# Performance work log

Measured on AMD Instinct MI355X. Metric: run time of the kernel, lower is better.

Reference implementation:

```python
import jax, jax.numpy as jnp
import numpy as np

H = 256  # hidden_size
I = 18   # input_size
B = 1024 # batch
T = 1024 # seq_len


def setup_inputs() -> dict:
    key = jax.random.key(0)
    ks = jax.random.split(key, 8)
    scale = 1.0 / np.sqrt(H)  # matches torch GRUCell uniform init scale roughly
    s = lambda k, shape: jax.random.normal(k, shape, dtype=jnp.float32) * scale
    return {
        "x": jax.random.normal(ks[0], (B, T, I), dtype=jnp.float32),
        # layer 0 GRUCell params (gate order r, z, n as in torch)
        "W_ih0": s(ks[1], (3 * H, I)),
        "W_hh0": s(ks[2], (3 * H, H)),
        "b_ih0": jnp.zeros((3 * H,), dtype=jnp.float32),
        "b_hh0": jnp.zeros((3 * H,), dtype=jnp.float32),
        # layer 1 GRUCell params
        "W_ih1": s(ks[3], (3 * H, H)),
        "W_hh1": s(ks[4], (3 * H, H)),
        "b_ih1": jnp.zeros((3 * H,), dtype=jnp.float32),
        "b_hh1": jnp.zeros((3 * H,), dtype=jnp.float32),
        "fc_w": s(ks[5], (1, H)),
        "fc_b": jnp.zeros((1,), dtype=jnp.float32),
    }


def _gru_cell(x, h, W_ih, W_hh, b_ih, b_hh):
    # torch.nn.GRUCell math, gate order (r, z, n)
    gi = x @ W_ih.T + b_ih  # (B, 3H)
    gh = h @ W_hh.T + b_hh  # (B, 3H)
    ir, iz, inn = jnp.split(gi, 3, axis=-1)
    hr, hz, hn = jnp.split(gh, 3, axis=-1)
    r = jax.nn.sigmoid(ir + hr)
    z = jax.nn.sigmoid(iz + hz)
    n = jnp.tanh(inn + r * hn)
    return (1.0 - z) * n + z * h


def reference(x, W_ih0, W_hh0, b_ih0, b_hh0, W_ih1, W_hh1, b_ih1, b_hh1, fc_w, fc_b):
    batch = x.shape[0]
    hid = W_hh0.shape[1]
    h_init = (jnp.zeros((batch, hid), dtype=x.dtype),
              jnp.zeros((batch, hid), dtype=x.dtype))
    xs = jnp.swapaxes(x, 0, 1)  # (T, B, I) for scan over time

    def step(carry, xt):
        h0, h1 = carry
        h0 = _gru_cell(xt, h0, W_ih0, W_hh0, b_ih0, b_hh0)
        h1 = _gru_cell(h0, h1, W_ih1, W_hh1, b_ih1, b_hh1)
        return (h0, h1), None

    (h0, h1), _ = jax.lax.scan(step, h_init, xs)
    return h1 @ fc_w.T + fc_b  # (B, 1)
```

## Files before the change

### kernel.cpp

```cpp
#include <hip/hip_runtime.h>

#define B_ 1024
#define T_ 1024
#define I_ 18
#define H_ 256
#define NCHUNK 16
#define NSLICE 16

typedef _Float16 f16;
typedef _Float16 f16x8 __attribute__((ext_vector_type(8)));
typedef float f32x4 __attribute__((ext_vector_type(4)));

#define MFMA16(a, b, c) __builtin_amdgcn_mfma_f32_16x16x32_f16((a), (b), (c), 0, 0, 0)
#define SB() __builtin_amdgcn_sched_barrier(0)

#define WF_FRAGS 75
#define WF_SLICE (WF_FRAGS * 512)
#define WF_TOTAL (NSLICE * WF_SLICE)
#define H_SLOT (NCHUNK * 8 * 4 * 512)
#define NFLAGS (NCHUNK * 4 * 32)

struct TrueT { static constexpr bool value = true; };
struct FalseT { static constexpr bool value = false; };

__device__ __forceinline__ int hoff(int chunk, int kt, int m) {
  return (((chunk * 8) + kt) * 4 + m) * 512;
}

__global__ void init_ws(f16* __restrict__ hb, int hcount, int* __restrict__ flg) {
  int i = blockIdx.x * blockDim.x + threadIdx.x;
  unsigned* p = (unsigned*)hb;
  for (int k = i; k < hcount / 2; k += gridDim.x * blockDim.x) p[k] = 0u;
  if (i < NFLAGS + 256 + 1) flg[i] = 0;
}

__global__ void prep_weights(const float* __restrict__ Wih0,
                             const float* __restrict__ Whh0,
                             const float* __restrict__ Wih1,
                             const float* __restrict__ Whh1,
                             f16* __restrict__ ws) {
  int tid = blockIdx.x * blockDim.x + threadIdx.x;
  if (tid >= NSLICE * WF_FRAGS * 64) return;
  int lane = tid & 63;
  int f = (tid >> 6) % WF_FRAGS;
  int s = tid / (WF_FRAGS * 64);
  int lrow = lane & 15, lgrp = lane >> 4;
  f16 v[8];
  if (f < 3) {
    int n = f * H_ + s * 16 + lrow;
#pragma unroll
    for (int j = 0; j < 8; ++j) {
      int k = lgrp * 8 + j;
      v[j] = (k < I_) ? (f16)Wih0[n * I_ + k] : (f16)0.f;
    }
  } else {
    int ff;
    const float* W;
    if (f < 27) { ff = f - 3;  W = Whh0; }
    else if (f < 51) { ff = f - 27; W = Wih1; }
    else { ff = f - 51; W = Whh1; }
    int g = ff >> 3, kt = ff & 7;
    int n = g * H_ + s * 16 + lrow;
    int kb = kt * 32 + lgrp * 8;
#pragma unroll
    for (int j = 0; j < 8; ++j) v[j] = (f16)W[n * H_ + kb + j];
  }
  *(f16x8*)(ws + ((size_t)s * WF_SLICE + f * 512 + lane * 8)) = *(f16x8*)v;
}

__device__ __forceinline__ float sigm(float v) {
  return __builtin_amdgcn_rcpf(1.f + __expf(-v));
}
__device__ __forceinline__ float tanh_fast(float v) {
  v = fmaxf(v, -15.f);
  float e = __expf(-2.f * v);
  return (1.f - e) * __builtin_amdgcn_rcpf(1.f + e);
}

template <bool FAST>
__device__ __forceinline__ f16x8 ldh(const f16* p) {
  f16x8 r;
  if (FAST)
    asm volatile("global_load_dwordx4 %0, %1, off nt" : "=&v"(r) : "v"(p));
  else
    asm volatile("global_load_dwordx4 %0, %1, off sc0 sc1" : "=&v"(r) : "v"(p));
  return r;
}
template <bool FAST>
__device__ __forceinline__ void sth(f16* p, f16 v) {
  unsigned u = (unsigned)__builtin_bit_cast(unsigned short, v);
  if (FAST)
    asm volatile("global_store_short %0, %1, off" ::"v"(p), "v"(u) : "memory");
  else
    asm volatile("global_store_short %0, %1, off sc0 sc1" ::"v"(p), "v"(u)
                 : "memory");
}
template <bool FAST>
__device__ __forceinline__ void stf(int* p, int v) {
  if (FAST)
    asm volatile("global_store_dword %0, %1, off" ::"v"(p), "v"(v) : "memory");
  else
    asm volatile("global_store_dword %0, %1, off sc0 sc1" ::"v"(p), "v"(v)
                 : "memory");
}
__device__ __forceinline__ int ld_sys(const int* p) {
  int r;
  asm volatile("global_load_dword %0, %1, off sc0 sc1\n\ts_waitcnt vmcnt(0)"
               : "=&v"(r) : "v"(p) : "memory");
  return r;
}
__device__ __forceinline__ void st_sys(int* p, int v) { stf<false>(p, v); }
__device__ __forceinline__ f32x4 ldx4(const float* p) {
  f32x4 r;
  asm volatile("global_load_dwordx4 %0, %1, off" : "=&v"(r) : "v"(p));
  return r;
}

__global__ __launch_bounds__(512, 2) void gru_main(
    const float* __restrict__ x, const float* __restrict__ bih0,
    const float* __restrict__ bhh0, const float* __restrict__ bih1,
    const float* __restrict__ bhh1, const float* __restrict__ fcw,
    const f16* __restrict__ wfr, f16* __restrict__ hb0, f16* __restrict__ hb1,
    float* __restrict__ part, int* __restrict__ flags, int* __restrict__ ids,
    int* __restrict__ dec, int hmask) {
  __shared__ f16 whh1_l[24 * 512];

  const int tid = threadIdx.x;
  const int wv = tid >> 6, lane = tid & 63;
  const int w = wv & 3;
  const bool isL0 = wv < 4;
  const int lrow = lane & 15, lgrp = lane >> 4;
  const int chunk = blockIdx.x & 15, slice = blockIdx.x >> 4;

  for (int i = tid; i < 24 * 64; i += 512)
    ((f16x8*)whh1_l)[i] =
        ((const f16x8*)(wfr + (size_t)slice * WF_SLICE + 51 * 512))[i];

  const int c = slice * 16 + lrow;
  const int* fpoll = flags + (chunk * 4 + w) * 32 + (lane & 31);
  const int rbase = chunk * 64 + w * 16;
  const int s_kt = slice >> 1;
  const int s_off = 128 * ((slice & 1) * 2 + (lrow >> 3)) + (lrow & 7);

  {
    unsigned xcc;
    asm volatile("s_getreg_b32 %0, hwreg(HW_REG_XCC_ID)" : "=s"(xcc));
    if (tid == 0) st_sys(ids + blockIdx.x, (int)xcc + 1);
    if (blockIdx.x == 0 && wv == 0) {
      int ok, guard = 0;
      for (;;) {
        int v0 = ld_sys(ids + lane * 4 + 0), v1 = ld_sys(ids + lane * 4 + 1);
        int v2 = ld_sys(ids + lane * 4 + 2), v3 = ld_sys(ids + lane * 4 + 3);
        ok = (v0 && v1 && v2 && v3);
        if (__all(ok)) { ok = 1; break; }
        if (++guard > (1 << 16)) { ok = 0; break; }
        __builtin_amdgcn_s_sleep(8);
      }
      int verdict = 1;
      if (ok) {
        int eq = 1;
        if (lane < 16) {
          int r0 = ld_sys(ids + lane);
          for (int s = 1; s < 16; ++s)
            eq &= (ld_sys(ids + s * 16 + lane) == r0);
        }
        verdict = __all(eq) ? 2 : 1;
      }
      if (lane == 0) st_sys(dec, verdict);
    }
  }
  int decision = 1;
  {
    int g = 0;
    for (;;) {
      int d = ld_sys(dec);
      if (d) { decision = d; break; }
      if (++g > (1 << 20)) break;
      __builtin_amdgcn_s_sleep(8);
    }
  }
  __syncthreads();

  if (isL0) {
    f16x8 wfA[27];
    {
      const f16* wb = wfr + (size_t)slice * WF_SLICE + lane * 8;
#pragma unroll
      for (int f = 0; f < 27; ++f) wfA[f] = *(const f16x8*)(wb + f * 512);
    }
    const float bR0 = bih0[c] + bhh0[c], bZ0 = bih0[H_ + c] + bhh0[H_ + c];
    const float bI0 = bih0[2 * H_ + c], bH0 = bhh0[2 * H_ + c];
    float h0r[4] = {0.f, 0.f, 0.f, 0.f};
    int* fpost0 = flags + (chunk * 4 + w) * 32 + slice;
    const float* xrow = x + (size_t)(rbase + lrow) * T_ * I_;
    const int o1 = (lgrp == 0) ? 0 : (lgrp == 1) ? 8 : (lgrp == 2) ? 14 : 0;
    const int o2 = (lgrp == 0) ? 4 : (lgrp == 1) ? 12 : 0;
    int dead = 0;

    auto loop0 = [&](auto FC) {
      constexpr bool F = decltype(FC)::value;
      asm volatile("s_waitcnt vmcnt(0)" ::: "memory");
      SB();
      f32x4 xA1 = ldx4(xrow + o1);
      f32x4 xA2 = ldx4(xrow + o2);
      for (int p = 0; p < T_; ++p) {
        if (p > 0 && !dead) {
          int tgt = (lane & 16) ? (p - hmask) : p;
          int guard = 0;
          for (;;) {
            int v;
            if (F)
              asm volatile("global_load_dword %0, %1, off nt"
                           : "=&v"(v) : "v"(fpoll));
            else
              asm volatile("global_load_dword %0, %1, off sc0 sc1"
                           : "=&v"(v) : "v"(fpoll));
            asm volatile("s_waitcnt vmcnt(0)" ::: "memory");
            if (__all(v >= tgt)) break;
            if (++guard > (1 << 18)) { dead = 1; break; }
          }
        }
        SB();
        __builtin_amdgcn_s_setprio(1);
        f16x8 ah0[8];
        {
          const f16* b0 = hb0 + (size_t)((p - 1) & hmask) * H_SLOT +
                          hoff(chunk, 0, w) + lane * 8;
#pragma unroll
          for (int kt = 0; kt < 8; ++kt) ah0[kt] = ldh<F>(b0 + kt * 2048);
        }
        SB();
        asm volatile("s_waitcnt vmcnt(4)" ::: "memory");
        SB();
        f16x8 ax;
        {
          float s0 = (lgrp == 2) ? xA1[2] : xA1[0];
          float s1 = (lgrp == 2) ? xA1[3] : xA1[1];
          ax[0] = (f16)s0;     ax[1] = (f16)s1;
          ax[2] = (f16)xA1[2]; ax[3] = (f16)xA1[3];
          ax[4] = (f16)xA2[0]; ax[5] = (f16)xA2[1];
          ax[6] = (f16)xA2[2]; ax[7] = (f16)xA2[3];
        }
        f32x4 aR = {bR0, bR0, bR0, bR0}, aZ = {bZ0, bZ0, bZ0, bZ0};
        f32x4 aI = {bI0, bI0, bI0, bI0}, aH = {bH0, bH0, bH0, bH0};
        aR = MFMA16(ax, wfA[0], aR);
        aZ = MFMA16(ax, wfA[1], aZ);
        aI = MFMA16(ax, wfA[2], aI);
#pragma unroll
        for (int kt = 0; kt < 4; ++kt) {
          aR = MFMA16(ah0[kt], wfA[3 + kt], aR);
          aZ = MFMA16(ah0[kt], wfA[11 + kt], aZ);
          aH = MFMA16(ah0[kt], wfA[19 + kt], aH);
        }
        SB();
        asm volatile("s_waitcnt vmcnt(0)" ::: "memory");
        SB();
#pragma unroll
        for (int kt = 4; kt < 8; ++kt) {
          aR = MFMA16(ah0[kt], wfA[3 + kt], aR);
          aZ = MFMA16(ah0[kt], wfA[11 + kt], aZ);
          aH = MFMA16(ah0[kt], wfA[19 + kt], aH);
        }
        {
          f16* d0 = hb0 + (size_t)(p & hmask) * H_SLOT +
                    hoff(chunk, s_kt, w) + s_off;
#pragma unroll
          for (int i = 0; i < 4; ++i) {
            float rr = sigm(aR[i]);
            float zz = sigm(aZ[i]);
            float nn = tanh_fast(aI[i] + rr * aH[i]);
            h0r[i] = (1.f - zz) * nn + zz * h0r[i];
            sth<F>(d0 + (lgrp * 4 + i) * 8, (f16)h0r[i]);
          }
        }
        SB();
        asm volatile("s_waitcnt vmcnt(0)" ::: "memory");
        SB();
        if (lane == 0) stf<F>(fpost0, p + 1);
        __builtin_amdgcn_s_setprio(0);
        {
          int tn = (p + 1 < T_) ? p + 1 : T_ - 1;
          const float* px = xrow + (size_t)tn * I_;
          xA1 = ldx4(px + o1);
          xA2 = ldx4(px + o2);
        }
      }
    };
    if (decision == 2) loop0(TrueT{});
    else loop0(FalseT{});
  } else {
    f16x8 wfB[24];
    {
      const f16* wb = wfr + (size_t)slice * WF_SLICE + 27 * 512 + lane * 8;
#pragma unroll
      for (int f = 0; f < 24; ++f) wfB[f] = *(const f16x8*)(wb + f * 512);
    }
    const float bR1 = bih1[c] + bhh1[c], bZ1 = bih1[H_ + c] + bhh1[H_ + c];
    const float bI1 = bih1[2 * H_ + c], bH1 = bhh1[2 * H_ + c];
    const float fw = fcw[c];
    float h1r[4] = {0.f, 0.f, 0.f, 0.f};
    int* fpost1 = flags + (chunk * 4 + w) * 32 + 16 + slice;
    int dead = 0;

    auto loop1 = [&](auto FC) {
      constexpr bool F = decltype(FC)::value;
      for (int p = 1; p <= T_; ++p) {
        if (!dead) {
          int tgt = (lane & 16) ? (p - 1) : p;
          int guard = 0;
          for (;;) {
            int v;
            if (F)
              asm volatile("global_load_dword %0, %1, off nt"
                           : "=&v"(v) : "v"(fpoll));
            else
              asm volatile("global_load_dword %0, %1, off sc0 sc1"
                           : "=&v"(v) : "v"(fpoll));
            asm volatile("s_waitcnt vmcnt(0)" ::: "memory");
            if (__all(v >= tgt)) break;
            if (++guard > (1 << 18)) { dead = 1; break; }
          }
        }
        SB();
        f16x8 ah0[8], ah1[8];
        {
          const f16* b0 = hb0 + (size_t)((p - 1) & hmask) * H_SLOT +
                          hoff(chunk, 0, w) + lane * 8;
          const f16* b1 = hb1 + (size_t)(p & 1) * H_SLOT +
                          hoff(chunk, 0, w) + lane * 8;
#pragma unroll
          for (int kt = 0; kt < 8; ++kt) ah0[kt] = ldh<F>(b0 + kt * 2048);
#pragma unroll
          for (int kt = 0; kt < 8; ++kt) ah1[kt] = ldh<F>(b1 + kt * 2048);
        }
        SB();
        asm volatile("s_waitcnt vmcnt(8)" ::: "memory");
        SB();
        f32x4 aR = {bR1, bR1, bR1, bR1}, aZ = {bZ1, bZ1, bZ1, bZ1};
        f32x4 aI = {bI1, bI1, bI1, bI1}, aH = {bH1, bH1, bH1, bH1};
#pragma unroll
        for (int kt = 0; kt < 8; ++kt) {
          aR = MFMA16(ah0[kt], wfB[kt], aR);
          aZ = MFMA16(ah0[kt], wfB[8 + kt], aZ);
          aI = MFMA16(ah0[kt], wfB[16 + kt], aI);
        }
        SB();
        asm volatile("s_waitcnt vmcnt(0)" ::: "memory");
        SB();
#pragma unroll
        for (int kt = 0; kt < 8; ++kt) {
          f16x8 br = *(const f16x8*)&whh1_l[(0 * 8 + kt) * 512 + lane * 8];
          f16x8 bz = *(const f16x8*)&whh1_l[(1 * 8 + kt) * 512 + lane * 8];
          f16x8 bn = *(const f16x8*)&whh1_l[(2 * 8 + kt) * 512 + lane * 8];
          aR = MFMA16(ah1[kt], br, aR);
          aZ = MFMA16(ah1[kt], bz, aZ);
          aH = MFMA16(ah1[kt], bn, aH);
        }
        {
          f16* d1 = hb1 + (size_t)((p - 1) & 1) * H_SLOT +
                    hoff(chunk, s_kt, w) + s_off;
#pragma unroll
          for (int i = 0; i < 4; ++i) {
            float rr = sigm(aR[i]);
            float zz = sigm(aZ[i]);
            float nn = tanh_fast(aI[i] + rr * aH[i]);
            h1r[i] = (1.f - zz) * nn + zz * h1r[i];
            sth<F>(d1 + (lgrp * 4 + i) * 8, (f16)h1r[i]);
          }
        }
        SB();
        asm volatile("s_waitcnt vmcnt(0)" ::: "memory");
        SB();
        if (lane == 0) stf<F>(fpost1, p);
      }
    };
    if (decision == 2) loop1(TrueT{});
    else loop1(FalseT{});

    float tmp[4];
#pragma unroll
    for (int i = 0; i < 4; ++i) {
      float v = h1r[i] * fw;
#pragma unroll
      for (int m = 1; m < 16; m <<= 1) v += __shfl_xor(v, m);
      tmp[i] = v;
    }
    if (lrow == 0) {
#pragma unroll
      for (int i = 0; i < 4; ++i)
        part[(size_t)(rbase + lgrp * 4 + i) * 16 + slice] = tmp[i];
    }
  }
}

__global__ void fc_reduce(const float* __restrict__ part,
                          const float* __restrict__ fcb,
                          float* __restrict__ out) {
  int r = blockIdx.x * blockDim.x + threadIdx.x;
  if (r < B_) {
    float s = fcb[0];
#pragma unroll
    for (int i = 0; i < 16; ++i) s += part[r * 16 + i];
    out[r] = s;
  }
}

extern "C" void kernel_launch(void* const* d_in, const int* in_sizes, int n_in,
                              void* d_out, int out_size, void* d_ws, size_t ws_size,
                              hipStream_t stream) {
  const float* x    = (const float*)d_in[0];
  const float* Wih0 = (const float*)d_in[1];
  const float* Whh0 = (const float*)d_in[2];
  const float* bih0 = (const float*)d_in[3];
  const float* bhh0 = (const float*)d_in[4];
  const float* Wih1 = (const float*)d_in[5];
  const float* Whh1 = (const float*)d_in[6];
  const float* bih1 = (const float*)d_in[7];
  const float* bhh1 = (const float*)d_in[8];
  const float* fcw  = (const float*)d_in[9];
  const float* fcb  = (const float*)d_in[10];

  size_t tail = 1024 * 16 * 4 + (NFLAGS + 256 + 8) * 4;
  size_t need4 = (size_t)(WF_TOTAL + 6 * H_SLOT) * 2 + tail;
  int hmask = (ws_size >= need4) ? 3 : 1;
  f16* wfr = (f16*)d_ws;
  f16* hb0 = wfr + WF_TOTAL;
  f16* hb1 = hb0 + (size_t)(hmask + 1) * H_SLOT;
  float* part = (float*)(hb1 + 2 * H_SLOT);
  int* flags = (int*)(part + 1024 * 16);
  int* ids = flags + NFLAGS;
  int* dec = ids + 256;
  int hcount = (hmask + 3) * H_SLOT;

  init_ws<<<1024, 256, 0, stream>>>(hb0, hcount, flags);
  prep_weights<<<300, 256, 0, stream>>>(Wih0, Whh0, Wih1, Whh1, wfr);
  gru_main<<<256, 512, 0, stream>>>(x, bih0, bhh0, bih1, bhh1, fcw, wfr, hb0,
                                    hb1, part, flags, ids, dec, hmask);
  fc_reduce<<<4, 256, 0, stream>>>(part, fcb, (float*)d_out);
}
```

Baseline: 2.005 ms.

## Fuse weight conversion into main kernel and split layer-1 waits for overlap

```diff
diff --git a/kernel.cpp b/kernel.cpp
--- a/kernel.cpp
+++ b/kernel.cpp
@@ -14,9 +14,6 @@
 #define MFMA16(a, b, c) __builtin_amdgcn_mfma_f32_16x16x32_f16((a), (b), (c), 0, 0, 0)
 #define SB() __builtin_amdgcn_sched_barrier(0)
 
-#define WF_FRAGS 75
-#define WF_SLICE (WF_FRAGS * 512)
-#define WF_TOTAL (NSLICE * WF_SLICE)
 #define H_SLOT (NCHUNK * 8 * 4 * 512)
 #define NFLAGS (NCHUNK * 4 * 32)
 
@@ -27,45 +24,11 @@
   return (((chunk * 8) + kt) * 4 + m) * 512;
 }
 
-__global__ void init_ws(f16* __restrict__ hb, int hcount, int* __restrict__ flg) {
+__global__ void init_ws(f16* __restrict__ hb, int* __restrict__ flg) {
   int i = blockIdx.x * blockDim.x + threadIdx.x;
   unsigned* p = (unsigned*)hb;
-  for (int k = i; k < hcount / 2; k += gridDim.x * blockDim.x) p[k] = 0u;
+  for (int k = i; k < 3 * H_SLOT; k += gridDim.x * blockDim.x) p[k] = 0u;
   if (i < NFLAGS + 256 + 1) flg[i] = 0;
-}
-
-__global__ void prep_weights(const float* __restrict__ Wih0,
-                             const float* __restrict__ Whh0,
-                             const float* __restrict__ Wih1,
-                             const float* __restrict__ Whh1,
-                             f16* __restrict__ ws) {
-  int tid = blockIdx.x * blockDim.x + threadIdx.x;
-  if (tid >= NSLICE * WF_FRAGS * 64) return;
-  int lane = tid & 63;
-  int f = (tid >> 6) % WF_FRAGS;
-  int s = tid / (WF_FRAGS * 64);
-  int lrow = lane & 15, lgrp = lane >> 4;
-  f16 v[8];
-  if (f < 3) {
-    int n = f * H_ + s * 16 + lrow;
-#pragma unroll
-    for (int j = 0; j < 8; ++j) {
-      int k = lgrp * 8 + j;
-      v[j] = (k < I_) ? (f16)Wih0[n * I_ + k] : (f16)0.f;
-    }
-  } else {
-    int ff;
-    const float* W;
-    if (f < 27) { ff = f - 3;  W = Whh0; }
-    else if (f < 51) { ff = f - 27; W = Wih1; }
-    else { ff = f - 51; W = Whh1; }
-    int g = ff >> 3, kt = ff & 7;
-    int n = g * H_ + s * 16 + lrow;
-    int kb = kt * 32 + lgrp * 8;
-#pragma unroll
-    for (int j = 0; j < 8; ++j) v[j] = (f16)W[n * H_ + kb + j];
-  }
-  *(f16x8*)(ws + ((size_t)s * WF_SLICE + f * 512 + lane * 8)) = *(f16x8*)v;
 }
 
 __device__ __forceinline__ float sigm(float v) {
@@ -75,6 +38,14 @@
   v = fmaxf(v, -15.f);
   float e = __expf(-2.f * v);
   return (1.f - e) * __builtin_amdgcn_rcpf(1.f + e);
+}
+__device__ __forceinline__ f16x8 cvt8(const float* q) {
+  const f32x4* a = (const f32x4*)q;
+  f32x4 u = a[0], v = a[1];
+  f16x8 r;
+  r[0] = (f16)u[0]; r[1] = (f16)u[1]; r[2] = (f16)u[2]; r[3] = (f16)u[3];
+  r[4] = (f16)v[0]; r[5] = (f16)v[1]; r[6] = (f16)v[2]; r[7] = (f16)v[3];
+  return r;
 }
 
 template <bool FAST>
@@ -103,6 +74,17 @@
     asm volatile("global_store_dword %0, %1, off sc0 sc1" ::"v"(p), "v"(v)
                  : "memory");
 }
+template <bool FAST>
+__device__ __forceinline__ int ldf(const int* p) {
+  int r;
+  if (FAST)
+    asm volatile("global_load_dword %0, %1, off nt\n\ts_waitcnt vmcnt(0)"
+                 : "=&v"(r) : "v"(p) : "memory");
+  else
+    asm volatile("global_load_dword %0, %1, off sc0 sc1\n\ts_waitcnt vmcnt(0)"
+                 : "=&v"(r) : "v"(p) : "memory");
+  return r;
+}
 __device__ __forceinline__ int ld_sys(const int* p) {
   int r;
   asm volatile("global_load_dword %0, %1, off sc0 sc1\n\ts_waitcnt vmcnt(0)"
@@ -117,12 +99,13 @@
 }
 
 __global__ __launch_bounds__(512, 2) void gru_main(
-    const float* __restrict__ x, const float* __restrict__ bih0,
+    const float* __restrict__ x, const float* __restrict__ Wih0,
+    const float* __restrict__ Whh0, const float* __restrict__ Wih1,
+    const float* __restrict__ Whh1, const float* __restrict__ bih0,
     const float* __restrict__ bhh0, const float* __restrict__ bih1,
     const float* __restrict__ bhh1, const float* __restrict__ fcw,
-    const f16* __restrict__ wfr, f16* __restrict__ hb0, f16* __restrict__ hb1,
-    float* __restrict__ part, int* __restrict__ flags, int* __restrict__ ids,
-    int* __restrict__ dec, int hmask) {
+    f16* __restrict__ hb0, f16* __restrict__ hb1, float* __restrict__ part,
+    int* __restrict__ flags, int* __restrict__ ids, int* __restrict__ dec) {
   __shared__ f16 whh1_l[24 * 512];
 
   const int tid = threadIdx.x;
@@ -131,12 +114,15 @@
   const bool isL0 = wv < 4;
   const int lrow = lane & 15, lgrp = lane >> 4;
   const int chunk = blockIdx.x & 15, slice = blockIdx.x >> 4;
-
-  for (int i = tid; i < 24 * 64; i += 512)
-    ((f16x8*)whh1_l)[i] =
-        ((const f16x8*)(wfr + (size_t)slice * WF_SLICE + 51 * 512))[i];
-
   const int c = slice * 16 + lrow;
+
+  for (int idx = tid; idx < 24 * 64; idx += 512) {
+    int f = idx >> 6, l = idx & 63;
+    int g = f >> 3, kt = f & 7;
+    int n = g * H_ + slice * 16 + (l & 15);
+    ((f16x8*)whh1_l)[idx] = cvt8(&Whh1[n * H_ + kt * 32 + (l >> 4) * 8]);
+  }
+
   const int* fpoll = flags + (chunk * 4 + w) * 32 + (lane & 31);
   const int rbase = chunk * 64 + w * 16;
   const int s_kt = slice >> 1;
@@ -183,11 +169,24 @@
 
   if (isL0) {
     f16x8 wfA[27];
-    {
-      const f16* wb = wfr + (size_t)slice * WF_SLICE + lane * 8;
-#pragma unroll
-      for (int f = 0; f < 27; ++f) wfA[f] = *(const f16x8*)(wb + f * 512);
+#pragma unroll
+    for (int g = 0; g < 3; ++g) {
+      int n = g * H_ + c;
+      f16 v[8];
+#pragma unroll
+      for (int j = 0; j < 8; ++j) {
+        int k = lgrp * 8 + j;
+        v[j] = (k < I_) ? (f16)Wih0[n * I_ + k] : (f16)0.f;
+      }
+      wfA[g] = *(f16x8*)v;
     }
+#pragma unroll
+    for (int g = 0; g < 3; ++g)
+#pragma unroll
+      for (int kt = 0; kt < 8; ++kt)
+        wfA[3 + g * 8 + kt] =
+            cvt8(&Whh0[(g * H_ + c) * H_ + kt * 32 + lgrp * 8]);
+
     const float bR0 = bih0[c] + bhh0[c], bZ0 = bih0[H_ + c] + bhh0[H_ + c];
     const float bI0 = bih0[2 * H_ + c], bH0 = bhh0[2 * H_ + c];
     float h0r[4] = {0.f, 0.f, 0.f, 0.f};
@@ -203,34 +202,27 @@
       SB();
       f32x4 xA1 = ldx4(xrow + o1);
       f32x4 xA2 = ldx4(xrow + o2);
+      asm volatile("s_waitcnt vmcnt(0)" ::: "memory");
+      SB();
       for (int p = 0; p < T_; ++p) {
+        __builtin_amdgcn_s_setprio(1);
         if (p > 0 && !dead) {
-          int tgt = (lane & 16) ? (p - hmask) : p;
           int guard = 0;
           for (;;) {
-            int v;
-            if (F)
-              asm volatile("global_load_dword %0, %1, off nt"
-                           : "=&v"(v) : "v"(fpoll));
-            else
-              asm volatile("global_load_dword %0, %1, off sc0 sc1"
-                           : "=&v"(v) : "v"(fpoll));
-            asm volatile("s_waitcnt vmcnt(0)" ::: "memory");
+            int v = ldf<F>(fpoll);
+            int tgt = (lane & 16) ? (p - 3) : p;
             if (__all(v >= tgt)) break;
             if (++guard > (1 << 18)) { dead = 1; break; }
           }
         }
         SB();
-        __builtin_amdgcn_s_setprio(1);
         f16x8 ah0[8];
         {
-          const f16* b0 = hb0 + (size_t)((p - 1) & hmask) * H_SLOT +
+          const f16* b0 = hb0 + (size_t)((p - 1) & 3) * H_SLOT +
                           hoff(chunk, 0, w) + lane * 8;
 #pragma unroll
           for (int kt = 0; kt < 8; ++kt) ah0[kt] = ldh<F>(b0 + kt * 2048);
         }
-        SB();
-        asm volatile("s_waitcnt vmcnt(4)" ::: "memory");
         SB();
         f16x8 ax;
         {
@@ -246,6 +238,9 @@
         aR = MFMA16(ax, wfA[0], aR);
         aZ = MFMA16(ax, wfA[1], aZ);
         aI = MFMA16(ax, wfA[2], aI);
+        SB();
+        asm volatile("s_waitcnt vmcnt(4)" ::: "memory");
+        SB();
 #pragma unroll
         for (int kt = 0; kt < 4; ++kt) {
           aR = MFMA16(ah0[kt], wfA[3 + kt], aR);
@@ -262,8 +257,8 @@
           aH = MFMA16(ah0[kt], wfA[19 + kt], aH);
         }
         {
-          f16* d0 = hb0 + (size_t)(p & hmask) * H_SLOT +
-                    hoff(chunk, s_kt, w) + s_off;
+          f16* d0 = hb0 + (size_t)(p & 3) * H_SLOT + hoff(chunk, s_kt, w) +
+                    s_off;
 #pragma unroll
           for (int i = 0; i < 4; ++i) {
             float rr = sigm(aR[i]);
@@ -273,28 +268,30 @@
             sth<F>(d0 + (lgrp * 4 + i) * 8, (f16)h0r[i]);
           }
         }
-        SB();
-        asm volatile("s_waitcnt vmcnt(0)" ::: "memory");
-        SB();
-        if (lane == 0) stf<F>(fpost0, p + 1);
-        __builtin_amdgcn_s_setprio(0);
         {
           int tn = (p + 1 < T_) ? p + 1 : T_ - 1;
           const float* px = xrow + (size_t)tn * I_;
           xA1 = ldx4(px + o1);
           xA2 = ldx4(px + o2);
         }
+        SB();
+        asm volatile("s_waitcnt vmcnt(2)" ::: "memory");
+        SB();
+        if (lane == 0) stf<F>(fpost0, p + 1);
+        __builtin_amdgcn_s_setprio(0);
       }
     };
     if (decision == 2) loop0(TrueT{});
     else loop0(FalseT{});
   } else {
     f16x8 wfB[24];
-    {
-      const f16* wb = wfr + (size_t)slice * WF_SLICE + 27 * 512 + lane * 8;
-#pragma unroll
-      for (int f = 0; f < 24; ++f) wfB[f] = *(const f16x8*)(wb + f * 512);
-    }
+#pragma unroll
+    for (int g = 0; g < 3; ++g)
+#pragma unroll
+      for (int kt = 0; kt < 8; ++kt)
+        wfB[g * 8 + kt] =
+            cvt8(&Wih1[(g * H_ + c) * H_ + kt * 32 + lgrp * 8]);
+
     const float bR1 = bih1[c] + bhh1[c], bZ1 = bih1[H_ + c] + bhh1[H_ + c];
     const float bI1 = bih1[2 * H_ + c], bH1 = bhh1[2 * H_ + c];
     const float fw = fcw[c];
@@ -306,47 +303,41 @@
       constexpr bool F = decltype(FC)::value;
       for (int p = 1; p <= T_; ++p) {
         if (!dead) {
-          int tgt = (lane & 16) ? (p - 1) : p;
           int guard = 0;
           for (;;) {
-            int v;
-            if (F)
-              asm volatile("global_load_dword %0, %1, off nt"
-                           : "=&v"(v) : "v"(fpoll));
-            else
-              asm volatile("global_load_dword %0, %1, off sc0 sc1"
-                           : "=&v"(v) : "v"(fpoll));
-            asm volatile("s_waitcnt vmcnt(0)" ::: "memory");
-            if (__all(v >= tgt)) break;
+            int v = ldf<F>(fpoll);
+            if (__all((lane & 16) ? (v >= p - 1) : 1)) break;
             if (++guard > (1 << 18)) { dead = 1; break; }
           }
         }
         SB();
-        f16x8 ah0[8], ah1[8];
-        {
-          const f16* b0 = hb0 + (size_t)((p - 1) & hmask) * H_SLOT +
-                          hoff(chunk, 0, w) + lane * 8;
+        f16x8 ah1[8];
+        {
           const f16* b1 = hb1 + (size_t)(p & 1) * H_SLOT +
                           hoff(chunk, 0, w) + lane * 8;
 #pragma unroll
+          for (int kt = 0; kt < 8; ++kt) ah1[kt] = ldh<F>(b1 + kt * 2048);
+        }
+        SB();
+        if (!dead) {
+          int guard = 0;
+          for (;;) {
+            int v = ldf<F>(fpoll);
+            if (__all((lane & 16) ? 1 : (v >= p))) break;
+            if (++guard > (1 << 18)) { dead = 1; break; }
+          }
+        }
+        SB();
+        f16x8 ah0[8];
+        {
+          const f16* b0 = hb0 + (size_t)((p - 1) & 3) * H_SLOT +
+                          hoff(chunk, 0, w) + lane * 8;
+#pragma unroll
           for (int kt = 0; kt < 8; ++kt) ah0[kt] = ldh<F>(b0 + kt * 2048);
-#pragma unroll
-          for (int kt = 0; kt < 8; ++kt) ah1[kt] = ldh<F>(b1 + kt * 2048);
-        }
-        SB();
-        asm volatile("s_waitcnt vmcnt(8)" ::: "memory");
+        }
         SB();
         f32x4 aR = {bR1, bR1, bR1, bR1}, aZ = {bZ1, bZ1, bZ1, bZ1};
         f32x4 aI = {bI1, bI1, bI1, bI1}, aH = {bH1, bH1, bH1, bH1};
-#pragma unroll
-        for (int kt = 0; kt < 8; ++kt) {
-          aR = MFMA16(ah0[kt], wfB[kt], aR);
-          aZ = MFMA16(ah0[kt], wfB[8 + kt], aZ);
-          aI = MFMA16(ah0[kt], wfB[16 + kt], aI);
-        }
-        SB();
-        asm volatile("s_waitcnt vmcnt(0)" ::: "memory");
-        SB();
 #pragma unroll
         for (int kt = 0; kt < 8; ++kt) {
           f16x8 br = *(const f16x8*)&whh1_l[(0 * 8 + kt) * 512 + lane * 8];
@@ -355,6 +346,15 @@
           aR = MFMA16(ah1[kt], br, aR);
           aZ = MFMA16(ah1[kt], bz, aZ);
           aH = MFMA16(ah1[kt], bn, aH);
+        }
+        SB();
+        asm volatile("s_waitcnt vmcnt(0)" ::: "memory");
+        SB();
+#pragma unroll
+        for (int kt = 0; kt < 8; ++kt) {
+          aR = MFMA16(ah0[kt], wfB[kt], aR);
+          aZ = MFMA16(ah0[kt], wfB[8 + kt], aZ);
+          aI = MFMA16(ah0[kt], wfB[16 + kt], aI);
         }
         {
           f16* d1 = hb1 + (size_t)((p - 1) & 1) * H_SLOT +
@@ -420,21 +420,16 @@
   const float* fcw  = (const float*)d_in[9];
   const float* fcb  = (const float*)d_in[10];
 
-  size_t tail = 1024 * 16 * 4 + (NFLAGS + 256 + 8) * 4;
-  size_t need4 = (size_t)(WF_TOTAL + 6 * H_SLOT) * 2 + tail;
-  int hmask = (ws_size >= need4) ? 3 : 1;
-  f16* wfr = (f16*)d_ws;
-  f16* hb0 = wfr + WF_TOTAL;
-  f16* hb1 = hb0 + (size_t)(hmask + 1) * H_SLOT;
-  float* part = (float*)(hb1 + 2 * H_SLOT);
+  f16* hb0 = (f16*)d_ws;
+  f16* hb1 = hb0 + (size_t)4 * H_SLOT;
+  float* part = (float*)(hb1 + (size_t)2 * H_SLOT);
   int* flags = (int*)(part + 1024 * 16);
   int* ids = flags + NFLAGS;
   int* dec = ids + 256;
-  int hcount = (hmask + 3) * H_SLOT;
-
-  init_ws<<<1024, 256, 0, stream>>>(hb0, hcount, flags);
-  prep_weights<<<300, 256, 0, stream>>>(Wih0, Whh0, Wih1, Whh1, wfr);
-  gru_main<<<256, 512, 0, stream>>>(x, bih0, bhh0, bih1, bhh1, fcw, wfr, hb0,
-                                    hb1, part, flags, ids, dec, hmask);
+
+  init_ws<<<1024, 256, 0, stream>>>(hb0, flags);
+  gru_main<<<256, 512, 0, stream>>>(x, Wih0, Whh0, Wih1, Whh1, bih0, bhh0,
+                                    bih1, bhh1, fcw, hb0, hb1, part, flags,
+                                    ids, dec);
   fc_reduce<<<4, 256, 0, stream>>>(part, fcb, (float*)d_out);
 }
```

New measurement: 1.905 ms. -5.0%, faster.
